# Performance work log

Measured on AMD Instinct MI355X. Metric: run time of the kernel, lower is better.

## Reference

```python
import jax, jax.numpy as jnp
import numpy as np

H, W, P = 480, 600, 2048
N = H * W
_IU = np.triu_indices(4)

def _conv(x, w, b, stride=1):
    y = jax.lax.conv_general_dilated(x, w, (stride, stride), 'SAME',
                                     dimension_numbers=('NCHW', 'OIHW', 'NCHW'))
    return y + b[None, :, None, None]

def _gn(x, scale, bias, groups=16, eps=1e-5):
    n, c, h, w = x.shape
    xg = x.reshape(n, groups, c // groups, h, w)
    mu = xg.mean(axis=(2, 3, 4), keepdims=True)
    var = xg.var(axis=(2, 3, 4), keepdims=True)
    xg = (xg - mu) * jax.lax.rsqrt(var + eps)
    return xg.reshape(n, c, h, w) * scale[None, :, None, None] + bias[None, :, None, None]

def _lrelu(x):
    return jnp.where(x >= 0, x, 0.2 * x)

def setup_inputs():
    key = jax.random.key(0)
    ks = jax.random.split(key, 16)
    def he(k, shape, fan_in):
        return jax.random.normal(k, shape, jnp.float32) * np.float32(np.sqrt(2.0 / fan_in))
    return {
        'depth': jax.random.normal(ks[0], (1, 1, H, W), jnp.float32),
        'pose': jax.random.normal(ks[1], (P, 2, 8), jnp.float32),
        'target_mask': (jax.random.uniform(ks[2], (1, 1, H, W)) > 0.5).astype(jnp.float32),
        'pairs': jax.random.randint(ks[3], (P, 2), 0, N),
        'conv1_w': he(ks[4], (32, 3, 3, 3), 3 * 9), 'conv1_b': jnp.zeros(32),
        'gn1_s': jnp.ones(32), 'gn1_b': jnp.zeros(32),
        'conv2_w': he(ks[5], (64, 32, 3, 3), 32 * 9), 'conv2_b': jnp.zeros(64),
        'gn2_s': jnp.ones(64), 'gn2_b': jnp.zeros(64),
        'conv3_w': he(ks[6], (64, 64, 3, 3), 64 * 9), 'conv3_b': jnp.zeros(64),
        'gn3_s': jnp.ones(64), 'gn3_b': jnp.zeros(64),
        'conv4_w': he(ks[7], (64, 96, 3, 3), 96 * 9), 'conv4_b': jnp.zeros(64),
        'gn4_s': jnp.ones(64), 'gn4_b': jnp.zeros(64),
        'gate_w': he(ks[8], (15, 64), 15), 'gate_b': jnp.zeros(64),
        'hid_w': he(ks[9], (64, 64), 64), 'hid_b': jnp.zeros(64),
        'out_w': he(ks[10], (64, 1), 64), 'out_b': jnp.zeros(1),
    }

def _forward(depth, pose, target_mask, params, pairs):
    (c1w, c1b, g1s, g1b, c2w, c2b, g2s, g2b, c3w, c3b, g3s, g3b,
     c4w, c4b, g4s, g4b, gw, gb, hw_, hb, ow, ob) = params
    idx = pairs[:, 0]
    hh, ww = idx // W, idx % W
    # vectorized replacement of the per-pair python-loop scatter
    attn = jnp.zeros((1, 1, H, W), jnp.float32).at[0, 0, hh, ww].set(1.0)
    std_depth = (depth - depth.mean()) * 10.0
    x = jnp.concatenate([std_depth, target_mask, attn], axis=1)  # [1,3,H,W]
    # res_unet backbone (encoder-decoder, GroupNorm, leaky-relu 0.2)
    c1 = _lrelu(_gn(_conv(x, c1w, c1b), g1s, g1b))               # [1,32,H,W]
    d1 = _lrelu(_gn(_conv(c1, c2w, c2b, stride=2), g2s, g2b))    # [1,64,H/2,W/2]
    bm = _lrelu(_gn(_conv(d1, c3w, c3b), g3s, g3b))              # [1,64,H/2,W/2]
    up = jax.image.resize(bm, (1, 64, H, W), method='nearest')
    u = jnp.concatenate([up, c1], axis=1)                         # [1,96,H,W]
    feats = _lrelu(_gn(_conv(u, c4w, c4b), g4s, g4b))            # [1,64,H,W]
    # vectorized per-pair gather
    fg = feats.reshape(64, N)[:, idx].T                           # [P,64]
    fg = jnp.broadcast_to(fg[:, None, :], (P, 2, 64))
    dg = std_depth.reshape(N)[idx]
    dg = jnp.broadcast_to(dg[:, None, None], (P, 2, 1))
    quat = pose[:, :, :4]
    fingers = pose[:, :, 4:7]
    trans = pose[:, :, 7:8]
    outer = quat[..., :, None] * quat[..., None, :]               # sign-invariant q_i*q_j
    enc = outer[..., _IU[0], _IU[1]]                              # [P,2,10]
    cond = jnp.concatenate([enc, fingers, trans, dg], axis=-1)    # [P,2,15]
    # ContextGate_1d: gated attention over gathered features
    gate = jax.nn.sigmoid(cond @ gw + gb)                         # [P,2,64]
    h = fg * gate
    h = h * jax.lax.rsqrt(jnp.sum(h * h, axis=-1, keepdims=True) + 1e-8)
    h = _lrelu(h @ hw_ + hb)
    return jax.nn.silu(h) @ ow + ob                               # [P,2,1]

def reference(depth, pose, target_mask, pairs, conv1_w, conv1_b, gn1_s, gn1_b,
              conv2_w, conv2_b, gn2_s, gn2_b, conv3_w, conv3_b, gn3_s, gn3_b,
              conv4_w, conv4_b, gn4_s, gn4_b, gate_w, gate_b, hid_w, hid_b,
              out_w, out_b):
    params = (conv1_w, conv1_b, gn1_s, gn1_b, conv2_w, conv2_b, gn2_s, gn2_b,
              conv3_w, conv3_b, gn3_s, gn3_b, conv4_w, conv4_b, gn4_s, gn4_b,
              gate_w, gate_b, hid_w, hid_b, out_w, out_b)
    return _forward(depth, pose, target_mask, params, pairs)
```

## Files before the change

### kernel.cpp

```cpp
#include <hip/hip_runtime.h>
#include <math.h>

#define HH 480
#define WW 600
#define NN (HH*WW)
#define PP 2048
#define H2 240
#define W2 300
#define N2 (H2*W2)

typedef __bf16  bf16x8  __attribute__((ext_vector_type(8)));
typedef __bf16  bf16x4  __attribute__((ext_vector_type(4)));
typedef float   f32x4   __attribute__((ext_vector_type(4)));
typedef ushort  ushort8 __attribute__((ext_vector_type(8)));

__device__ __forceinline__ ushort f2b(float f) {
    unsigned u = __float_as_uint(f);
    unsigned r = (u + 0x7FFF + ((u >> 16) & 1)) >> 16;
    return (ushort)r;
}
__device__ __forceinline__ float b2f(ushort u) {
    return __uint_as_float(((unsigned)u) << 16);
}

__device__ __forceinline__ void gl_lds16(const ushort* g, ushort* l) {
    __builtin_amdgcn_global_load_lds(
        (const __attribute__((address_space(1))) unsigned int*)g,
        (__attribute__((address_space(3))) unsigned int*)l, 16, 0, 0);
}

constexpr size_t alup(size_t x) { return (x + 65535) & ~(size_t)65535; }
constexpr size_t OFF_X    = 65536;
constexpr size_t OFF_C1R  = alup(OFF_X    + 3UL*NN*4);
constexpr size_t OFF_C1N  = alup(OFF_C1R  + 32UL*NN*2);
constexpr size_t OFF_RW2R = alup(OFF_C1N  + 482UL*602*32*2 + 65536);
constexpr size_t OFF_RW2N = alup(OFF_RW2R + 64UL*N2*2);
constexpr size_t OFF_RW3R = alup(OFF_RW2N + 242UL*302*64*2 + 65536);
constexpr size_t OFF_RW3N = alup(OFF_RW3R + 64UL*N2*2);
constexpr size_t OFF_WB2  = alup(OFF_RW3N + 242UL*302*64*2 + 65536);
constexpr size_t OFF_WB3  = alup(OFF_WB2 + 36864UL);
constexpr size_t OFF_WB4  = alup(OFF_WB3 + 73728UL);
constexpr size_t OFF_SLOT = alup(OFF_WB4 + 110592UL);
constexpr size_t OFF_CMP  = alup(OFF_SLOT + (size_t)NN*4);

__global__ void k_sum(const float* __restrict__ d, float* __restrict__ ws) {
    float s = 0.f;
    for (int i = blockIdx.x*blockDim.x + threadIdx.x; i < NN; i += gridDim.x*blockDim.x)
        s += d[i];
    #pragma unroll
    for (int o = 32; o; o >>= 1) s += __shfl_down(s, o, 64);
    __shared__ float sm[4];
    int wid = threadIdx.x >> 6;
    if ((threadIdx.x & 63) == 0) sm[wid] = s;
    __syncthreads();
    if (threadIdx.x == 0) {
        float t = 0.f;
        for (int w = 0; w < (int)(blockDim.x >> 6); ++w) t += sm[w];
        atomicAdd(ws, t);
    }
}

__global__ void k_buildx(const float* __restrict__ depth, const float* __restrict__ mask,
                         const float* __restrict__ ws, float* __restrict__ x) {
    int i = blockIdx.x*blockDim.x + threadIdx.x;
    if (i >= NN) return;
    float mean = ws[0] * (1.0f/NN);
    x[i]        = (depth[i] - mean) * 10.0f;
    x[NN + i]   = mask[i];
    x[2*NN + i] = 0.f;
}

__global__ void k_scatter(const int* __restrict__ pairs, float* __restrict__ x) {
    int p = blockIdx.x*blockDim.x + threadIdx.x;
    if (p < PP) x[2*NN + pairs[2*p]] = 1.0f;
}

__global__ void k_slot(const int* __restrict__ pairs, int* __restrict__ slotmap) {
    int p = blockIdx.x*blockDim.x + threadIdx.x;
    if (p < PP) slotmap[pairs[2*p]] = p;
}

__global__ void k_borders(ushort* __restrict__ c1n, ushort* __restrict__ rw2n,
                          ushort* __restrict__ rw3n) {
    int i = blockIdx.x*256 + threadIdx.x;
    ushort* buf; int Hp, Wp, upp, j = i;
    if (i < 8656)            { buf = c1n;  Hp = 482; Wp = 602; upp = 4; }
    else if (i < 17328)      { buf = rw2n; Hp = 242; Wp = 302; upp = 8; j = i - 8656; }
    else if (i < 26000)      { buf = rw3n; Hp = 242; Wp = 302; upp = 8; j = i - 17328; }
    else return;
    int px = j / upp, oct = j - (j/upp)*upp;
    int y, x;
    if (px < Wp)        { y = 0;      x = px; }
    else if (px < 2*Wp) { y = Hp - 1; x = px - Wp; }
    else { int s = px - 2*Wp; y = 1 + (s >> 1); x = (s & 1) ? Wp - 1 : 0; }
    ushort8 z = {};
    *(ushort8*)&buf[((size_t)y*Wp + x)*(upp*8) + oct*8] = z;
}

__global__ void k_wcvt(const float* __restrict__ w, ushort* __restrict__ dst, int NCH) {
    int e = blockIdx.x*256 + threadIdx.x;
    int total = 9*NCH*64*32;
    if (e >= total) return;
    int k  = e & 31;
    int co = (e >> 5) & 63;
    int rest = e >> 11;
    int c = rest % NCH;
    int t = rest / NCH;
    dst[e] = f2b(w[(co*(NCH*32) + c*32 + k)*9 + t]);
}

template<int TCO>
__global__ __launch_bounds__(256) void k_conv1(const float* __restrict__ in,
        const float* __restrict__ w, const float* __restrict__ bias,
        ushort* __restrict__ outb, float* __restrict__ stat) {
    __shared__ float sred[4][16];
    int wv   = threadIdx.x >> 6;
    int lane = threadIdx.x & 63;
    int x    = blockIdx.x*64 + lane;
    int y    = blockIdx.y*4 + wv;
    int co0  = blockIdx.z*TCO;
    bool valid = x < WW;
    int  xb   = x - 1;
    bool xint = (xb >= 0) && (xb + 2 < WW);

    float iv[3][3][3];
    #pragma unroll
    for (int ci = 0; ci < 3; ++ci) {
        const float* ip = in + (long)ci*NN;
        #pragma unroll
        for (int dy = 0; dy < 3; ++dy) {
            int iy = y + dy - 1;
            if ((unsigned)iy < (unsigned)HH) {
                const float* rp = ip + (long)iy*WW + xb;
                if (xint) { iv[ci][dy][0]=rp[0]; iv[ci][dy][1]=rp[1]; iv[ci][dy][2]=rp[2]; }
                else {
                    #pragma unroll
                    for (int dx = 0; dx < 3; ++dx) {
                        int ix = xb + dx;
                        iv[ci][dy][dx] = ((unsigned)ix < (unsigned)WW) ? ip[(long)iy*WW+ix] : 0.f;
                    }
                }
            } else {
                iv[ci][dy][0] = iv[ci][dy][1] = iv[ci][dy][2] = 0.f;
            }
        }
    }

    float acc[TCO];
    #pragma unroll
    for (int c = 0; c < TCO; ++c) acc[c] = bias[co0+c];
    #pragma unroll
    for (int ci = 0; ci < 3; ++ci) {
        const float* wp = w + ((long)co0*3 + ci)*9;
        #pragma unroll
        for (int c = 0; c < TCO; ++c)
            #pragma unroll
            for (int k = 0; k < 9; ++k)
                acc[c] += iv[ci][k/3][k%3] * wp[(long)c*3*9 + k];
    }

    float s[TCO/2], s2[TCO/2];
    #pragma unroll
    for (int j = 0; j < TCO/2; ++j) { s[j] = 0.f; s2[j] = 0.f; }
    if (valid) {
        bf16x8 p0, p1;
        #pragma unroll
        for (int j = 0; j < 8; ++j) { p0[j] = (__bf16)acc[j]; p1[j] = (__bf16)acc[8+j]; }
        ushort* op = outb + (size_t)(y*WW + x)*32 + co0;
        *(ushort8*)op     = __builtin_bit_cast(ushort8, p0);
        *(ushort8*)(op+8) = __builtin_bit_cast(ushort8, p1);
        #pragma unroll
        for (int j = 0; j < TCO/2; ++j) {
            float a = acc[2*j], b = acc[2*j+1];
            s[j]  = a + b;
            s2[j] = a*a + b*b;
        }
    }

    #pragma unroll
    for (int o = 1; o < 64; o <<= 1)
        #pragma unroll
        for (int j = 0; j < TCO/2; ++j) {
            s[j]  += __shfl_xor(s[j],  o, 64);
            s2[j] += __shfl_xor(s2[j], o, 64);
        }
    float v = 0.f;
    #pragma unroll
    for (int j = 0; j < TCO/2; ++j) {
        v = (lane == j)         ? s[j]  : v;
        v = (lane == j + TCO/2) ? s2[j] : v;
    }
    if (lane < TCO) sred[wv][lane] = v;
    __syncthreads();
    if (threadIdx.x < TCO) {
        float t = sred[0][threadIdx.x] + sred[1][threadIdx.x]
                + sred[2][threadIdx.x] + sred[3][threadIdx.x];
        int g0 = co0 >> 1;
        int addr = (threadIdx.x < TCO/2) ? (g0 + threadIdx.x)
                                         : (16 + g0 + threadIdx.x - TCO/2);
        atomicAdd(&stat[addr], t);
    }
}

template<int C, int CHPER>
__global__ __launch_bounds__(256) void k_gnpack(const ushort* __restrict__ raw,
        ushort* __restrict__ outp, const float* __restrict__ gs,
        const float* __restrict__ gb, const float* __restrict__ st,
        int Wwd, float cnt) {
    constexpr int UPP = C/8;
    int y = blockIdx.y;
    int e = blockIdx.x*256 + threadIdx.x;
    if (e >= Wwd*UPP) return;
    int x   = e / UPP;
    int oct = e - x*UPP;
    int c0  = oct*8;
    ushort8 r = *(const ushort8*)&raw[((size_t)y*Wwd + x)*C + c0];
    bf16x8 o;
    #pragma unroll
    for (int j = 0; j < 8; ++j) {
        int c = c0 + j, g = c / CHPER;
        float mu  = st[g] / cnt;
        float var = st[16+g] / cnt - mu*mu;
        float rs  = rsqrtf(var + 1e-5f);
        float v = (b2f(r[j]) - mu) * rs * gs[c] + gb[c];
        o[j] = (__bf16)fmaxf(v, 0.2f*v);
    }
    *(ushort8*)&outp[(((size_t)y + 1)*(Wwd + 2) + x + 1)*C + c0] = __builtin_bit_cast(ushort8, o);
}

template<int MODE>
__global__ __launch_bounds__(256) void k_sconv(
        const ushort* __restrict__ inA, const ushort* __restrict__ inB,
        const ushort* __restrict__ wb, const float* __restrict__ bias,
        ushort* __restrict__ outb,
        const int* __restrict__ slotmap, float* __restrict__ compact,
        float* __restrict__ stat) {
    constexpr int Wo   = (MODE==4) ? WW : W2;
    constexpr int NCH  = (MODE==2) ? 1 : (MODE==3) ? 2 : 3;
    constexpr int NPT  = (MODE==4) ? 4 : 2;
    constexpr int ROWS = (MODE==2) ? 9 : 6;
    constexpr int PXS  = (MODE==3) ? 36 : 68;
    constexpr int UNITS = ROWS*PXS*4;
    constexpr int NLD  = (UNITS + 255)/256;
    __shared__ __align__(16) ushort sh[UNITS*8];
    __shared__ float sred[4][16][2];

    int w    = threadIdx.x >> 6;
    int lane = threadIdx.x & 63;
    int lm   = lane & 15;
    int lg   = lane >> 4;
    int y0   = blockIdx.y*4;
    int x0   = blockIdx.x*(NPT*16);
    int y    = y0 + w;
    int iy0  = (MODE==2) ? 2*y0 : y0 - 1;
    int ix0  = (MODE==2) ? 2*x0 : x0 - 1;

    f32x4 acc[4][NPT];
    #pragma unroll
    for (int ct = 0; ct < 4; ++ct)
        #pragma unroll
        for (int pt = 0; pt < NPT; ++pt) acc[ct][pt] = 0.f;

    #pragma unroll
    for (int kc = 0; kc < NCH; ++kc) {
        if (kc) __syncthreads();
        #pragma unroll
        for (int i = 0; i < NLD; ++i) {
            int u = i*256 + (int)threadIdx.x;
            if (u < UNITS) {
                int r  = u / (PXS*4);
                int rm = u - r*(PXS*4);
                int px = rm >> 2;
                int qp = rm & 3;
                int q  = (MODE==2) ? (qp ^ ((px>>1)&3) ^ ((px>>3)&3))
                                   : (qp ^ (px&3) ^ ((px>>2)&3));
                int iy = iy0 + r;
                int ix = ix0 + px;
                const ushort* sp;
                if (MODE==2)      sp = inA + ((size_t)(iy+1)*602 + (ix+1))*32 + q*8;
                else if (MODE==3) sp = inA + ((size_t)(iy+1)*302 + (ix+1))*64 + kc*32 + q*8;
                else if (kc < 2)  sp = inA + ((size_t)((iy>>1)+1)*302 + ((ix>>1)+1))*64 + kc*32 + q*8;
                else              sp = inB + ((size_t)(iy+1)*602 + (ix+1))*32 + q*8;
                gl_lds16(sp, &sh[(size_t)u*8]);
            }
        }
        __syncthreads();
        #pragma unroll
        for (int t = 0; t < 9; ++t) {
            const int dy = t/3, dx = t - 3*(t/3);
            const ushort* wp = wb + (size_t)((t*NCH + kc)*64)*32;
            bf16x8 a[4];
            #pragma unroll
            for (int ct = 0; ct < 4; ++ct)
                a[ct] = *(const bf16x8*)(wp + (ct*16 + lm)*32 + lg*8);
            int rr = (MODE==2) ? (2*w + dy) : (w + dy);
            #pragma unroll
            for (int pt = 0; pt < NPT; ++pt) {
                int pxl = (MODE==2) ? (2*lm + pt*32 + dx) : (pt*16 + lm + dx);
                int swz = (MODE==2) ? (((pxl>>1)&3) ^ ((pxl>>3)&3))
                                    : ((pxl&3) ^ ((pxl>>2)&3));
                int unit = (rr*PXS + pxl)*4 + (lg ^ swz);
                bf16x8 b = *(const bf16x8*)&sh[(size_t)unit*8];
                #pragma unroll
                for (int ct = 0; ct < 4; ++ct)
                    acc[ct][pt] = __builtin_amdgcn_mfma_f32_16x16x32_bf16(a[ct], b, acc[ct][pt], 0, 0, 0);
            }
        }
    }

    if (MODE != 4) {
        #pragma unroll
        for (int ct = 0; ct < 4; ++ct) {
            float s = 0.f, s2 = 0.f;
            #pragma unroll
            for (int pt = 0; pt < NPT; ++pt) {
                int pxg = x0 + pt*16 + lm;
                bool vld = pxg < Wo;
                bf16x4 pk;
                #pragma unroll
                for (int reg = 0; reg < 4; ++reg) {
                    int co = ct*16 + lg*4 + reg;
                    float v = acc[ct][pt][reg] + bias[co];
                    pk[reg] = (__bf16)v;
                    if (vld) { s += v; s2 += v*v; }
                }
                if (vld)
                    *(bf16x4*)(outb + (size_t)(y*Wo + pxg)*64 + ct*16 + lg*4) = pk;
            }
            #pragma unroll
            for (int o = 1; o < 16; o <<= 1) {
                s  += __shfl_xor(s,  o, 64);
                s2 += __shfl_xor(s2, o, 64);
            }
            if (lm == 0) { sred[w][ct*4+lg][0] = s; sred[w][ct*4+lg][1] = s2; }
        }
    } else {
        int slots[4];
        #pragma unroll
        for (int pt = 0; pt < 4; ++pt) {
            int pxg = x0 + pt*16 + lm;
            slots[pt] = (pxg < Wo) ? slotmap[(size_t)y*Wo + pxg] : -1;
        }
        #pragma unroll
        for (int ct = 0; ct < 4; ++ct) {
            float s = 0.f, s2 = 0.f;
            #pragma unroll
            for (int pt = 0; pt < 4; ++pt) {
                int pxg = x0 + pt*16 + lm;
                bool vld = pxg < Wo;
                f32x4 r;
                #pragma unroll
                for (int reg = 0; reg < 4; ++reg) {
                    int co = ct*16 + lg*4 + reg;
                    float v = acc[ct][pt][reg] + bias[co];
                    r[reg] = v;
                    if (vld) { s += v; s2 += v*v; }
                }
                if (slots[pt] >= 0)
                    *(f32x4*)(compact + (size_t)slots[pt]*64 + ct*16 + lg*4) = r;
            }
            #pragma unroll
            for (int o = 1; o < 16; o <<= 1) {
                s  += __shfl_xor(s,  o, 64);
                s2 += __shfl_xor(s2, o, 64);
            }
            if (lm == 0) { sred[w][ct*4+lg][0] = s; sred[w][ct*4+lg][1] = s2; }
        }
    }
    __syncthreads();
    if (threadIdx.x < 32) {
        int g = threadIdx.x >> 1, k = threadIdx.x & 1;
        float t = sred[0][g][k] + sred[1][g][k] + sred[2][g][k] + sred[3][g][k];
        atomicAdd(&stat[k*16 + g], t);
    }
}

__global__ void k_mlp(const float* __restrict__ pose, const float* __restrict__ sd,
                      const int* __restrict__ pairs, const int* __restrict__ slotmap,
                      const float* __restrict__ compact,
                      const float* __restrict__ g4s, const float* __restrict__ g4b,
                      const float* __restrict__ st4,
                      const float* __restrict__ gw, const float* __restrict__ gb,
                      const float* __restrict__ hw, const float* __restrict__ hb,
                      const float* __restrict__ ow, const float* __restrict__ ob,
                      float* __restrict__ out) {
    int wid  = threadIdx.x >> 6;
    int lane = threadIdx.x & 63;
    int t = blockIdx.x*4 + wid;
    int p = t >> 1;
    const float* pp = pose + t*8;
    float q0=pp[0], q1=pp[1], q2=pp[2], q3=pp[3];
    float f0=pp[4], f1=pp[5], f2=pp[6], tr=pp[7];
    int idx = pairs[2*p];
    float dg = sd[idx];
    float cond[15] = {q0*q0,q0*q1,q0*q2,q0*q3,q1*q1,q1*q2,q1*q3,q2*q2,q2*q3,q3*q3,
                      f0,f1,f2,tr,dg};
    float acc = gb[lane];
    #pragma unroll
    for (int k = 0; k < 15; ++k) acc += cond[k]*gw[k*64+lane];
    float gate = 1.f/(1.f+expf(-acc));
    int slot = slotmap[idx];
    float raw = compact[(size_t)slot*64 + lane];
    int   g4  = lane >> 2;
    float cnt = 4.0f * (float)NN;
    float mu  = st4[g4] / cnt;
    float var = st4[16+g4] / cnt - mu*mu;
    float rs  = rsqrtf(var + 1e-5f);
    float fv  = (raw - mu) * rs * g4s[lane] + g4b[lane];
    float fg  = fv >= 0.f ? fv : 0.2f*fv;
    float h = fg*gate;
    float ss = h*h;
    #pragma unroll
    for (int o = 32; o; o >>= 1) ss += __shfl_xor(ss, o, 64);
    h *= rsqrtf(ss + 1e-8f);
    __shared__ float hs[4][64];
    hs[wid][lane] = h;
    __syncthreads();
    float a2 = hb[lane];
    #pragma unroll 8
    for (int d = 0; d < 64; ++d) a2 += hs[wid][d]*hw[d*64+lane];
    float h2 = a2 >= 0.f ? a2 : 0.2f*a2;
    float si = h2 / (1.f+expf(-h2));
    float v = si * ow[lane];
    #pragma unroll
    for (int o = 32; o; o >>= 1) v += __shfl_xor(v, o, 64);
    if (lane == 0) out[t] = v + ob[0];
}

extern "C" void kernel_launch(void* const* d_in, const int* in_sizes, int n_in,
                              void* d_out, int out_size, void* d_ws, size_t ws_size,
                              hipStream_t stream) {
    const float* depth = (const float*)d_in[0];
    const float* pose  = (const float*)d_in[1];
    const float* mask  = (const float*)d_in[2];
    const int*   pairs = (const int*)  d_in[3];
    const float* c1w = (const float*)d_in[4];  const float* c1b = (const float*)d_in[5];
    const float* g1s = (const float*)d_in[6];  const float* g1b = (const float*)d_in[7];
    const float* c2w = (const float*)d_in[8];  const float* c2b = (const float*)d_in[9];
    const float* g2s = (const float*)d_in[10]; const float* g2b = (const float*)d_in[11];
    const float* c3w = (const float*)d_in[12]; const float* c3b = (const float*)d_in[13];
    const float* g3s = (const float*)d_in[14]; const float* g3b = (const float*)d_in[15];
    const float* c4w = (const float*)d_in[16]; const float* c4b = (const float*)d_in[17];
    const float* g4s = (const float*)d_in[18]; const float* g4b = (const float*)d_in[19];
    const float* gw  = (const float*)d_in[20]; const float* gb  = (const float*)d_in[21];
    const float* hw_ = (const float*)d_in[22]; const float* hb  = (const float*)d_in[23];
    const float* ow  = (const float*)d_in[24]; const float* ob  = (const float*)d_in[25];

    char* base = (char*)d_ws;
    float*  stats = (float*) base;
    float*  X    = (float*) (base + OFF_X);
    ushort* C1R  = (ushort*)(base + OFF_C1R);
    ushort* C1N  = (ushort*)(base + OFF_C1N);
    ushort* RW2R = (ushort*)(base + OFF_RW2R);
    ushort* RW2N = (ushort*)(base + OFF_RW2N);
    ushort* RW3R = (ushort*)(base + OFF_RW3R);
    ushort* RW3N = (ushort*)(base + OFF_RW3N);
    ushort* WB2  = (ushort*)(base + OFF_WB2);
    ushort* WB3  = (ushort*)(base + OFF_WB3);
    ushort* WB4  = (ushort*)(base + OFF_WB4);
    int*    SLOT = (int*)   (base + OFF_SLOT);
    float*  CMP  = (float*) (base + OFF_CMP);
    float* st1 = stats + 16;
    float* st2 = stats + 64;
    float* st3 = stats + 112;
    float* st4 = stats + 160;

    hipMemsetAsync(d_ws, 0, 1024, stream);
    hipMemsetAsync(SLOT, 0xFF, (size_t)NN*4, stream);

    k_sum    <<<1024, 256, 0, stream>>>(depth, stats);
    k_buildx <<<(NN+255)/256, 256, 0, stream>>>(depth, mask, stats, X);
    k_scatter<<<(PP+255)/256, 256, 0, stream>>>(pairs, X);
    k_slot   <<<(PP+255)/256, 256, 0, stream>>>(pairs, SLOT);
    k_borders<<<102, 256, 0, stream>>>(C1N, RW2N, RW3N);
    k_wcvt   <<< 72, 256, 0, stream>>>(c2w, WB2, 1);
    k_wcvt   <<<144, 256, 0, stream>>>(c3w, WB3, 2);
    k_wcvt   <<<216, 256, 0, stream>>>(c4w, WB4, 3);

    k_conv1<16><<<dim3(10, 120, 2), 256, 0, stream>>>(X, c1w, c1b, C1R, st1);
    k_gnpack<32,2><<<dim3(10, 480), 256, 0, stream>>>(C1R, C1N, g1s, g1b, st1, WW, 2.0f*NN);

    k_sconv<2><<<dim3(10, 60), 256, 0, stream>>>(C1N, nullptr, WB2, c2b,
        RW2R, nullptr, nullptr, st2);
    k_gnpack<64,4><<<dim3(10, 240), 256, 0, stream>>>(RW2R, RW2N, g2s, g2b, st2, W2, 4.0f*N2);

    k_sconv<3><<<dim3(10, 60), 256, 0, stream>>>(RW2N, nullptr, WB3, c3b,
        RW3R, nullptr, nullptr, st3);
    k_gnpack<64,4><<<dim3(10, 240), 256, 0, stream>>>(RW3R, RW3N, g3s, g3b, st3, W2, 4.0f*N2);

    k_sconv<4><<<dim3(10, 120), 256, 0, stream>>>(RW3N, C1N, WB4, c4b,
        nullptr, SLOT, CMP, st4);

    k_mlp<<<(2*PP)/4, 256, 0, stream>>>(pose, X, pairs, SLOT, CMP, g4s, g4b, st4,
                                        gw, gb, hw_, hb, ow, ob, (float*)d_out);
}
```

Baseline: 317.3 us.

## Double-buffer channel-chunk staging in sconv, split stride-2 conv, fuse pair kernels

Conv3/conv4 now stage the input halo tile for each channel chunk into one of two LDS buffers and use explicit vmcnt waits plus barriers, so global-to-LDS loads for the next chunk overlap MFMA work on the current one. Conv4 tile width drops from 64 to 32 pixels (grid 19x120), giving more blocks and a smaller LDS footprint. The stride-2 conv2 gets its own specialized kernel with a simpler swizzle and a trimmed halo width. The scatter and slot-map kernels are merged into one launch. In exchange there is more halo redundancy per output pixel for conv4, extra barrier traffic, and a changed LDS swizzle whose bank-conflict behaviour is untested.

```diff
diff --git a/kernel.cpp b/kernel.cpp
--- a/kernel.cpp
+++ b/kernel.cpp
@@ -70,14 +70,14 @@
     x[2*NN + i] = 0.f;
 }
 
-__global__ void k_scatter(const int* __restrict__ pairs, float* __restrict__ x) {
+__global__ void k_pairs(const int* __restrict__ pairs, float* __restrict__ x,
+                        int* __restrict__ slotmap) {
     int p = blockIdx.x*blockDim.x + threadIdx.x;
-    if (p < PP) x[2*NN + pairs[2*p]] = 1.0f;
-}
-
-__global__ void k_slot(const int* __restrict__ pairs, int* __restrict__ slotmap) {
-    int p = blockIdx.x*blockDim.x + threadIdx.x;
-    if (p < PP) slotmap[pairs[2*p]] = p;
+    if (p < PP) {
+        int idx = pairs[2*p];
+        x[2*NN + idx] = 1.0f;
+        slotmap[idx] = p;
+    }
 }
 
 __global__ void k_borders(ushort* __restrict__ c1n, ushort* __restrict__ rw2n,
@@ -228,21 +228,115 @@
     *(ushort8*)&outp[(((size_t)y + 1)*(Wwd + 2) + x + 1)*C + c0] = __builtin_bit_cast(ushort8, o);
 }
 
+__global__ __launch_bounds__(256) void k_sconv2(
+        const ushort* __restrict__ inA, const ushort* __restrict__ wb,
+        const float* __restrict__ bias, ushort* __restrict__ outb,
+        float* __restrict__ stat) {
+    constexpr int ROWS = 9, PXS = 66;
+    constexpr int UNITS = ROWS*PXS*4;
+    constexpr int NLD = (UNITS + 255)/256;
+    __shared__ __align__(16) ushort sh[UNITS*8];
+    __shared__ float sred[4][16][2];
+
+    int w    = threadIdx.x >> 6;
+    int lane = threadIdx.x & 63;
+    int lm   = lane & 15;
+    int lg   = lane >> 4;
+    int y0   = blockIdx.y*4;
+    int x0   = blockIdx.x*32;
+    int y    = y0 + w;
+    int iy0  = 2*y0;
+    int ix0  = 2*x0;
+
+    f32x4 acc[4][2];
+    #pragma unroll
+    for (int ct = 0; ct < 4; ++ct)
+        #pragma unroll
+        for (int pt = 0; pt < 2; ++pt) acc[ct][pt] = 0.f;
+
+    #pragma unroll
+    for (int i = 0; i < NLD; ++i) {
+        int u = i*256 + (int)threadIdx.x;
+        if (u < UNITS) {
+            int r  = u / (PXS*4);
+            int rm = u - r*(PXS*4);
+            int px = rm >> 2;
+            int q  = (rm & 3) ^ ((px>>1)&3);
+            int iy = iy0 + r;
+            int ix = ix0 + px;
+            const ushort* sp = inA + ((size_t)(iy+1)*602 + (ix+1))*32 + q*8;
+            gl_lds16(sp, &sh[(size_t)u*8]);
+        }
+    }
+    __syncthreads();
+
+    #pragma unroll
+    for (int t = 0; t < 9; ++t) {
+        const int dy = t/3, dx = t - 3*(t/3);
+        const ushort* wp = wb + (size_t)(t*64)*32;
+        bf16x8 a[4];
+        #pragma unroll
+        for (int ct = 0; ct < 4; ++ct)
+            a[ct] = *(const bf16x8*)(wp + (ct*16 + lm)*32 + lg*8);
+        int rr = 2*w + dy;
+        #pragma unroll
+        for (int pt = 0; pt < 2; ++pt) {
+            int pxl = 2*lm + pt*32 + dx;
+            int unit = (rr*PXS + pxl)*4 + (lg ^ ((pxl>>1)&3));
+            bf16x8 b = *(const bf16x8*)&sh[(size_t)unit*8];
+            #pragma unroll
+            for (int ct = 0; ct < 4; ++ct)
+                acc[ct][pt] = __builtin_amdgcn_mfma_f32_16x16x32_bf16(a[ct], b, acc[ct][pt], 0, 0, 0);
+        }
+    }
+
+    #pragma unroll
+    for (int ct = 0; ct < 4; ++ct) {
+        float s = 0.f, s2 = 0.f;
+        #pragma unroll
+        for (int pt = 0; pt < 2; ++pt) {
+            int pxg = x0 + pt*16 + lm;
+            bool vld = pxg < W2;
+            bf16x4 pk;
+            #pragma unroll
+            for (int reg = 0; reg < 4; ++reg) {
+                int co = ct*16 + lg*4 + reg;
+                float v = acc[ct][pt][reg] + bias[co];
+                pk[reg] = (__bf16)v;
+                if (vld) { s += v; s2 += v*v; }
+            }
+            if (vld)
+                *(bf16x4*)(outb + (size_t)(y*W2 + pxg)*64 + ct*16 + lg*4) = pk;
+        }
+        #pragma unroll
+        for (int o = 1; o < 16; o <<= 1) {
+            s  += __shfl_xor(s,  o, 64);
+            s2 += __shfl_xor(s2, o, 64);
+        }
+        if (lm == 0) { sred[w][ct*4+lg][0] = s; sred[w][ct*4+lg][1] = s2; }
+    }
+    __syncthreads();
+    if (threadIdx.x < 32) {
+        int g = threadIdx.x >> 1, k = threadIdx.x & 1;
+        float t = sred[0][g][k] + sred[1][g][k] + sred[2][g][k] + sred[3][g][k];
+        atomicAdd(&stat[k*16 + g], t);
+    }
+}
+
 template<int MODE>
-__global__ __launch_bounds__(256) void k_sconv(
+__global__ __launch_bounds__(256) void k_sconvP(
         const ushort* __restrict__ inA, const ushort* __restrict__ inB,
         const ushort* __restrict__ wb, const float* __restrict__ bias,
         ushort* __restrict__ outb,
         const int* __restrict__ slotmap, float* __restrict__ compact,
         float* __restrict__ stat) {
     constexpr int Wo   = (MODE==4) ? WW : W2;
-    constexpr int NCH  = (MODE==2) ? 1 : (MODE==3) ? 2 : 3;
-    constexpr int NPT  = (MODE==4) ? 4 : 2;
-    constexpr int ROWS = (MODE==2) ? 9 : 6;
-    constexpr int PXS  = (MODE==3) ? 36 : 68;
+    constexpr int NCH  = (MODE==3) ? 2 : 3;
+    constexpr int ROWS = 6, PXS = 36;
     constexpr int UNITS = ROWS*PXS*4;
-    constexpr int NLD  = (UNITS + 255)/256;
-    __shared__ __align__(16) ushort sh[UNITS*8];
+    constexpr int NLDP = 4;
+    constexpr int BUFU = NLDP*256;
+    __shared__ __align__(16) ushort sh[2*BUFU*8];
     __shared__ float sred[4][16][2];
 
     int w    = threadIdx.x >> 6;
@@ -250,41 +344,38 @@
     int lm   = lane & 15;
     int lg   = lane >> 4;
     int y0   = blockIdx.y*4;
-    int x0   = blockIdx.x*(NPT*16);
+    int x0   = blockIdx.x*32;
     int y    = y0 + w;
-    int iy0  = (MODE==2) ? 2*y0 : y0 - 1;
-    int ix0  = (MODE==2) ? 2*x0 : x0 - 1;
-
-    f32x4 acc[4][NPT];
+    int iy0  = y0 - 1;
+    int ix0  = x0 - 1;
+
+    f32x4 acc[4][2];
     #pragma unroll
     for (int ct = 0; ct < 4; ++ct)
         #pragma unroll
-        for (int pt = 0; pt < NPT; ++pt) acc[ct][pt] = 0.f;
-
-    #pragma unroll
-    for (int kc = 0; kc < NCH; ++kc) {
-        if (kc) __syncthreads();
-        #pragma unroll
-        for (int i = 0; i < NLD; ++i) {
-            int u = i*256 + (int)threadIdx.x;
-            if (u < UNITS) {
-                int r  = u / (PXS*4);
-                int rm = u - r*(PXS*4);
-                int px = rm >> 2;
-                int qp = rm & 3;
-                int q  = (MODE==2) ? (qp ^ ((px>>1)&3) ^ ((px>>3)&3))
-                                   : (qp ^ (px&3) ^ ((px>>2)&3));
-                int iy = iy0 + r;
-                int ix = ix0 + px;
-                const ushort* sp;
-                if (MODE==2)      sp = inA + ((size_t)(iy+1)*602 + (ix+1))*32 + q*8;
-                else if (MODE==3) sp = inA + ((size_t)(iy+1)*302 + (ix+1))*64 + kc*32 + q*8;
-                else if (kc < 2)  sp = inA + ((size_t)((iy>>1)+1)*302 + ((ix>>1)+1))*64 + kc*32 + q*8;
-                else              sp = inB + ((size_t)(iy+1)*602 + (ix+1))*32 + q*8;
-                gl_lds16(sp, &sh[(size_t)u*8]);
-            }
-        }
-        __syncthreads();
+        for (int pt = 0; pt < 2; ++pt) acc[ct][pt] = 0.f;
+
+    auto STAGE = [&](int buf, int kc) {
+        #pragma unroll
+        for (int i = 0; i < NLDP; ++i) {
+            int u  = i*256 + (int)threadIdx.x;
+            int uc = (u < UNITS) ? u : 0;
+            int r  = uc / (PXS*4);
+            int rm = uc - r*(PXS*4);
+            int px = rm >> 2;
+            int q  = (rm & 3) ^ ((px>>1)&3);
+            int iy = iy0 + r;
+            int ix = ix0 + px;
+            const ushort* sp;
+            if (MODE==3)      sp = inA + ((size_t)(iy+1)*302 + (ix+1))*64 + kc*32 + q*8;
+            else if (kc < 2)  sp = inA + ((size_t)((iy>>1)+1)*302 + ((ix>>1)+1))*64 + kc*32 + q*8;
+            else              sp = inB + ((size_t)(iy+1)*602 + (ix+1))*32 + q*8;
+            gl_lds16(sp, &sh[((size_t)buf*BUFU + (size_t)u)*8]);
+        }
+    };
+
+    auto COMPUTE = [&](int buf, int kc) {
+        const ushort* shb = &sh[(size_t)buf*BUFU*8];
         #pragma unroll
         for (int t = 0; t < 9; ++t) {
             const int dy = t/3, dx = t - 3*(t/3);
@@ -293,27 +384,45 @@
             #pragma unroll
             for (int ct = 0; ct < 4; ++ct)
                 a[ct] = *(const bf16x8*)(wp + (ct*16 + lm)*32 + lg*8);
-            int rr = (MODE==2) ? (2*w + dy) : (w + dy);
-            #pragma unroll
-            for (int pt = 0; pt < NPT; ++pt) {
-                int pxl = (MODE==2) ? (2*lm + pt*32 + dx) : (pt*16 + lm + dx);
-                int swz = (MODE==2) ? (((pxl>>1)&3) ^ ((pxl>>3)&3))
-                                    : ((pxl&3) ^ ((pxl>>2)&3));
-                int unit = (rr*PXS + pxl)*4 + (lg ^ swz);
-                bf16x8 b = *(const bf16x8*)&sh[(size_t)unit*8];
+            int rr = w + dy;
+            #pragma unroll
+            for (int pt = 0; pt < 2; ++pt) {
+                int pxl = pt*16 + lm + dx;
+                int unit = (rr*PXS + pxl)*4 + (lg ^ ((pxl>>1)&3));
+                bf16x8 b = *(const bf16x8*)&shb[(size_t)unit*8];
                 #pragma unroll
                 for (int ct = 0; ct < 4; ++ct)
                     acc[ct][pt] = __builtin_amdgcn_mfma_f32_16x16x32_bf16(a[ct], b, acc[ct][pt], 0, 0, 0);
             }
         }
-    }
-
-    if (MODE != 4) {
+    };
+
+    STAGE(0, 0);
+    STAGE(1, 1);
+    asm volatile("s_waitcnt vmcnt(%0)" :: "n"(NLDP) : "memory");
+    __builtin_amdgcn_s_barrier();
+    COMPUTE(0, 0);
+    if constexpr (NCH == 2) {
+        asm volatile("s_waitcnt vmcnt(0)" ::: "memory");
+        __builtin_amdgcn_s_barrier();
+        COMPUTE(1, 1);
+    } else {
+        __builtin_amdgcn_s_barrier();
+        STAGE(0, 2);
+        asm volatile("s_waitcnt vmcnt(%0)" :: "n"(NLDP) : "memory");
+        __builtin_amdgcn_s_barrier();
+        COMPUTE(1, 1);
+        asm volatile("s_waitcnt vmcnt(0)" ::: "memory");
+        __builtin_amdgcn_s_barrier();
+        COMPUTE(0, 2);
+    }
+
+    if (MODE == 3) {
         #pragma unroll
         for (int ct = 0; ct < 4; ++ct) {
             float s = 0.f, s2 = 0.f;
             #pragma unroll
-            for (int pt = 0; pt < NPT; ++pt) {
+            for (int pt = 0; pt < 2; ++pt) {
                 int pxg = x0 + pt*16 + lm;
                 bool vld = pxg < Wo;
                 bf16x4 pk;
@@ -335,9 +444,9 @@
             if (lm == 0) { sred[w][ct*4+lg][0] = s; sred[w][ct*4+lg][1] = s2; }
         }
     } else {
-        int slots[4];
-        #pragma unroll
-        for (int pt = 0; pt < 4; ++pt) {
+        int slots[2];
+        #pragma unroll
+        for (int pt = 0; pt < 2; ++pt) {
             int pxg = x0 + pt*16 + lm;
             slots[pt] = (pxg < Wo) ? slotmap[(size_t)y*Wo + pxg] : -1;
         }
@@ -345,7 +454,7 @@
         for (int ct = 0; ct < 4; ++ct) {
             float s = 0.f, s2 = 0.f;
             #pragma unroll
-            for (int pt = 0; pt < 4; ++pt) {
+            for (int pt = 0; pt < 2; ++pt) {
                 int pxg = x0 + pt*16 + lm;
                 bool vld = pxg < Wo;
                 f32x4 r;
@@ -470,8 +579,7 @@
 
     k_sum    <<<1024, 256, 0, stream>>>(depth, stats);
     k_buildx <<<(NN+255)/256, 256, 0, stream>>>(depth, mask, stats, X);
-    k_scatter<<<(PP+255)/256, 256, 0, stream>>>(pairs, X);
-    k_slot   <<<(PP+255)/256, 256, 0, stream>>>(pairs, SLOT);
+    k_pairs  <<<(PP+255)/256, 256, 0, stream>>>(pairs, X, SLOT);
     k_borders<<<102, 256, 0, stream>>>(C1N, RW2N, RW3N);
     k_wcvt   <<< 72, 256, 0, stream>>>(c2w, WB2, 1);
     k_wcvt   <<<144, 256, 0, stream>>>(c3w, WB3, 2);
@@ -480,15 +588,14 @@
     k_conv1<16><<<dim3(10, 120, 2), 256, 0, stream>>>(X, c1w, c1b, C1R, st1);
     k_gnpack<32,2><<<dim3(10, 480), 256, 0, stream>>>(C1R, C1N, g1s, g1b, st1, WW, 2.0f*NN);
 
-    k_sconv<2><<<dim3(10, 60), 256, 0, stream>>>(C1N, nullptr, WB2, c2b,
-        RW2R, nullptr, nullptr, st2);
+    k_sconv2<<<dim3(10, 60), 256, 0, stream>>>(C1N, WB2, c2b, RW2R, st2);
     k_gnpack<64,4><<<dim3(10, 240), 256, 0, stream>>>(RW2R, RW2N, g2s, g2b, st2, W2, 4.0f*N2);
 
-    k_sconv<3><<<dim3(10, 60), 256, 0, stream>>>(RW2N, nullptr, WB3, c3b,
+    k_sconvP<3><<<dim3(10, 60), 256, 0, stream>>>(RW2N, nullptr, WB3, c3b,
         RW3R, nullptr, nullptr, st3);
     k_gnpack<64,4><<<dim3(10, 240), 256, 0, stream>>>(RW3R, RW3N, g3s, g3b, st3, W2, 4.0f*N2);
 
-    k_sconv<4><<<dim3(10, 120), 256, 0, stream>>>(RW3N, C1N, WB4, c4b,
+    k_sconvP<4><<<dim3(19, 120), 256, 0, stream>>>(RW3N, C1N, WB4, c4b,
         nullptr, SLOT, CMP, st4);
 
     k_mlp<<<(2*PP)/4, 256, 0, stream>>>(pose, X, pairs, SLOT, CMP, g4s, g4b, st4,
```

After: 339.5 us. 1.07x slower.
